# Kernel optimization log

Measured on AMD Instinct MI355X. Metric: run time of the kernel, lower is better.

The kernel has to match this reference:

```python
import jax, jax.numpy as jnp
import numpy as np
from jax import lax

B, S, N, C = 8, 256, 64, 64  # batch, time=freq (square, required by concat), n, c
EPS = 1e-3  # keras BatchNormalization / LayerNormalization default epsilon


def _conv(x, w, b):
    # 3x3 stride-1 SAME conv, NHWC / HWIO
    return lax.conv_general_dilated(x, w, (1, 1), 'SAME',
                                    dimension_numbers=('NHWC', 'HWIO', 'NHWC')) + b


def _bn(x, g, b):
    # training-mode batch norm: stats over batch+spatial axes
    m = jnp.mean(x, (0, 1, 2))
    v = jnp.var(x, (0, 1, 2))
    return (x - m) * lax.rsqrt(v + EPS) * g + b


def _ln(x, g, b):
    m = jnp.mean(x, -1, keepdims=True)
    v = jnp.var(x, -1, keepdims=True)
    return (x - m) * lax.rsqrt(v + EPS) * g + b


def _attn(q, k, v):
    # q,k,v: [B, C, L, D]; scaled dot-product attention over axis L
    d = q.shape[-1]
    s = jnp.einsum('bcid,bcjd->bcij', q, k) / jnp.sqrt(jnp.float32(d))
    a = jax.nn.softmax(s, axis=-1)
    return jnp.einsum('bcij,bcjd->bcid', a, v)


def setup_inputs():
    key = jax.random.key(0)
    ks = jax.random.split(key, 16)
    w = lambda k, sh: jax.random.normal(k, sh, jnp.float32) * 0.05
    inp = {
        'inputs': jax.random.normal(ks[0], (B, S, S, N), jnp.float32),
        'wq': w(ks[1], (3, 3, N, C)), 'bq': jnp.zeros((C,), jnp.float32),
        'wk': w(ks[2], (3, 3, N, C)), 'bk': jnp.zeros((C,), jnp.float32),
        'wv': w(ks[3], (3, 3, N, C)), 'bv': jnp.zeros((C,), jnp.float32),
        'gq': jnp.ones((C,), jnp.float32), 'betaq': jnp.zeros((C,), jnp.float32),
        'gk': jnp.ones((C,), jnp.float32), 'betak': jnp.zeros((C,), jnp.float32),
        'gv': jnp.ones((C,), jnp.float32), 'betav': jnp.zeros((C,), jnp.float32),
        'wc': w(ks[4], (3, 3, 2 * S, N)), 'bc': jnp.zeros((N,), jnp.float32),
        'ln_g': jnp.ones((N,), jnp.float32), 'ln_b': jnp.zeros((N,), jnp.float32),
        'w1': w(ks[5], (3, 3, N, N)), 'b1': jnp.zeros((N,), jnp.float32),
        'g1': jnp.ones((N,), jnp.float32), 'beta1': jnp.zeros((N,), jnp.float32),
        'w2': w(ks[6], (3, 3, N, N)), 'b2': jnp.zeros((N,), jnp.float32),
        'g2': jnp.ones((N,), jnp.float32), 'beta2': jnp.zeros((N,), jnp.float32),
    }
    return inp


def reference(inputs, wq, bq, wk, bk, wv, bv, gq, betaq, gk, betak, gv, betav,
              wc, bc, ln_g, ln_b, w1, b1, g1, beta1, w2, b2, g2, beta2):
    q = _bn(_conv(inputs, wq, bq), gq, betaq)
    k = _bn(_conv(inputs, wk, bk), gk, betak)
    v = _bn(_conv(inputs, wv, bv), gv, betav)
    # axial attention: over time ([B,C,T,F]) and over frequency ([B,C,F,T])
    qt, kt, vt = (jnp.transpose(t, (0, 3, 1, 2)) for t in (q, k, v))
    qf, kf, vf = (jnp.transpose(t, (0, 3, 2, 1)) for t in (q, k, v))
    at = _attn(qt, kt, vt)  # [B, C, S, S]
    af = _attn(qf, kf, vf)  # [B, C, S, S]
    out = jnp.concatenate([at, af], axis=-1)  # [B, C, S, 2S] treated as NHWC
    out = _ln(_conv(out, wc, bc), ln_g, ln_b)  # [B, C, S, N]
    f1 = _bn(jax.nn.relu(_conv(out, w1, b1)), g1, beta1)
    f2 = _bn(jax.nn.relu(_conv(f1, w2, b2)), g2, beta2)
    return f2
```

## Files before the change

kernel.cpp:

```cpp
#include <hip/hip_runtime.h>
#include <hip/hip_bf16.h>

typedef unsigned short u16;
typedef u16 us8 __attribute__((ext_vector_type(8)));
typedef u16 us4 __attribute__((ext_vector_type(4)));
typedef __bf16 bfx8 __attribute__((ext_vector_type(8)));
typedef float f32x4 __attribute__((ext_vector_type(4)));

#define EPS 1e-3f

__device__ __forceinline__ float bf2f(u16 u){ unsigned x = ((unsigned)u)<<16; return __builtin_bit_cast(float, x); }
__device__ __forceinline__ u16 f2bu(float f){ __hip_bfloat16 h = __float2bfloat16(f); return __builtin_bit_cast(u16, h); }
__device__ __forceinline__ bfx8 ldb8(const u16* p){ return __builtin_bit_cast(bfx8, *(const us8*)p); }

__global__ __launch_bounds__(256) void prepw_k(const float* __restrict__ src, u16* __restrict__ dst, int CI)
{
  int total = 9*CI*64;
  int idx = blockIdx.x*256 + threadIdx.x;
  if (idx < total){
    int ci = idx % CI; int rest = idx / CI; int co = rest & 63; int t = rest >> 6;
    dst[idx] = f2bu(src[((size_t)t*CI + ci)*64 + co]);
  }
}

__global__ __launch_bounds__(768) void conv_qkv_f32_k(
    const float* __restrict__ in,
    const u16* __restrict__ WtQ, const u16* __restrict__ WtK, const u16* __restrict__ WtV,
    const float* __restrict__ bq, const float* __restrict__ bk, const float* __restrict__ bv,
    u16* __restrict__ qo, u16* __restrict__ ko, u16* __restrict__ vo)
{
  int b = blockIdx.z, y0 = blockIdx.y*2, x0 = blockIdx.x*128;
  int tid = threadIdx.x, lane = tid & 63, wid = tid >> 6;
  int g3 = wid >> 2, wid4 = wid & 3;
  int l15 = lane & 15, lhi = lane >> 4;
  __shared__ u16 lds[4*130*64];

  for (int idx = tid; idx < 8320; idx += 768){
    int row = idx >> 4, c4 = idx & 15;
    int yy = row / 130, xx = row - yy*130;
    int gy = y0 + yy - 1, gx = x0 + xx - 1;
    us4 v = {0,0,0,0};
    if ((unsigned)gy < 256u && (unsigned)gx < 256u){
      float4 f = *(const float4*)(in + ((((size_t)b*256 + gy)*256 + gx)<<6) + c4*4);
      v[0] = f2bu(f.x); v[1] = f2bu(f.y); v[2] = f2bu(f.z); v[3] = f2bu(f.w);
    }
    *(us4*)(lds + row*64 + ((c4*4) ^ ((xx&7)<<3))) = v;
  }
  __syncthreads();

  const u16*  Wt   = (g3==0) ? WtQ : (g3==1) ? WtK : WtV;
  const float* bias = (g3==0) ? bq  : (g3==1) ? bk  : bv;
  u16*        outp = (g3==0) ? qo  : (g3==1) ? ko  : vo;

  f32x4 acc[2][2][4];
#pragma unroll
  for (int nf=0; nf<4; nf++){
    float bb = bias[nf*16 + l15];
#pragma unroll
    for (int ry=0; ry<2; ry++){
      acc[ry][0][nf] = (f32x4){bb,bb,bb,bb};
      acc[ry][1][nf] = (f32x4){bb,bb,bb,bb};
    }
  }
  int xbase = wid4*32;
#pragma unroll
  for (int ky=0; ky<3; ky++)
#pragma unroll
    for (int kx=0; kx<3; kx++){
      int t = ky*3 + kx;
      bfx8 bfr[2][4];
#pragma unroll
      for (int ks=0; ks<2; ks++)
#pragma unroll
        for (int nf=0; nf<4; nf++)
          bfr[ks][nf] = ldb8(Wt + ((t*64 + nf*16 + l15)<<6) + ks*32 + lhi*8);
#pragma unroll
      for (int ks=0; ks<2; ks++)
#pragma unroll
        for (int ry=0; ry<2; ry++)
#pragma unroll
          for (int mt=0; mt<2; mt++){
            int xx = xbase + mt*16 + l15 + kx;
            bfx8 a = ldb8(lds + ((ry+ky)*130 + xx)*64 + ((ks*32 + lhi*8) ^ ((xx&7)<<3)));
#pragma unroll
            for (int nf=0; nf<4; nf++)
              acc[ry][mt][nf] = __builtin_amdgcn_mfma_f32_16x16x32_bf16(a, bfr[ks][nf], acc[ry][mt][nf], 0,0,0);
          }
    }
#pragma unroll
  for (int ry=0; ry<2; ry++)
#pragma unroll
    for (int mt=0; mt<2; mt++)
#pragma unroll
      for (int nf=0; nf<4; nf++)
#pragma unroll
        for (int r=0; r<4; r++){
          int x = x0 + xbase + mt*16 + lhi*4 + r;
          outp[((((size_t)b*256 + (y0+ry))*256 + x)<<6) + nf*16 + l15] = f2bu(acc[ry][mt][nf][r]);
        }
}

template<bool RELU>
__global__ __launch_bounds__(256) void conv2_mfma_k(
    const u16* __restrict__ in, const u16* __restrict__ Wt, const float* __restrict__ bias,
    u16* __restrict__ out)
{
  int b = blockIdx.z, y0 = blockIdx.y*2, x0 = blockIdx.x*128;
  int tid = threadIdx.x, lane = tid & 63, wid = tid >> 6;
  int l15 = lane & 15, lhi = lane >> 4;
  __shared__ u16 lds[4*130*64];

  for (int idx = tid; idx < 4160; idx += 256){
    int row = idx >> 3, ch = idx & 7;
    int yy = row / 130, xx = row - yy*130;
    int gy = y0 + yy - 1, gx = x0 + xx - 1;
    us8 v = {0,0,0,0,0,0,0,0};
    if ((unsigned)gy < 64u && (unsigned)gx < 256u)
      v = *(const us8*)(in + ((((size_t)b*64 + gy)*256 + gx)<<6) + ch*8);
    *(us8*)(lds + row*64 + ((ch*8) ^ ((xx&7)<<3))) = v;
  }
  __syncthreads();

  f32x4 acc[2][2][4];
#pragma unroll
  for (int nf=0; nf<4; nf++){
    float bb = bias[nf*16 + l15];
#pragma unroll
    for (int ry=0; ry<2; ry++){
      acc[ry][0][nf] = (f32x4){bb,bb,bb,bb};
      acc[ry][1][nf] = (f32x4){bb,bb,bb,bb};
    }
  }
  int xbase = wid*32;
#pragma unroll
  for (int ky=0; ky<3; ky++)
#pragma unroll
    for (int kx=0; kx<3; kx++){
      int t = ky*3 + kx;
      bfx8 bfr[2][4];
#pragma unroll
      for (int ks=0; ks<2; ks++)
#pragma unroll
        for (int nf=0; nf<4; nf++)
          bfr[ks][nf] = ldb8(Wt + ((t*64 + nf*16 + l15)<<6) + ks*32 + lhi*8);
#pragma unroll
      for (int ks=0; ks<2; ks++)
#pragma unroll
        for (int ry=0; ry<2; ry++)
#pragma unroll
          for (int mt=0; mt<2; mt++){
            int xx = xbase + mt*16 + l15 + kx;
            bfx8 a = ldb8(lds + ((ry+ky)*130 + xx)*64 + ((ks*32 + lhi*8) ^ ((xx&7)<<3)));
#pragma unroll
            for (int nf=0; nf<4; nf++)
              acc[ry][mt][nf] = __builtin_amdgcn_mfma_f32_16x16x32_bf16(a, bfr[ks][nf], acc[ry][mt][nf], 0,0,0);
          }
    }
#pragma unroll
  for (int ry=0; ry<2; ry++)
#pragma unroll
    for (int mt=0; mt<2; mt++)
#pragma unroll
      for (int nf=0; nf<4; nf++)
#pragma unroll
        for (int r=0; r<4; r++){
          int x = x0 + xbase + mt*16 + lhi*4 + r;
          float vv = acc[ry][mt][nf][r];
          if (RELU) vv = fmaxf(vv, 0.f);
          out[((((size_t)b*64 + (y0+ry))*256 + x)<<6) + nf*16 + l15] = f2bu(vv);
        }
}

__global__ __launch_bounds__(256) void conv_cat_ln_k(
    const u16* __restrict__ in, const u16* __restrict__ Wt, const float* __restrict__ bias,
    const float* __restrict__ lng, const float* __restrict__ lnb, u16* __restrict__ out)
{
  int b = blockIdx.z, y0 = blockIdx.y*2, x0 = blockIdx.x*128;
  int tid = threadIdx.x, lane = tid & 63, wid = tid >> 6;
  int l15 = lane & 15, lhi = lane >> 4;
  __shared__ u16 lds[4*130*64];

  f32x4 acc[2][2][4];
#pragma unroll
  for (int nf=0; nf<4; nf++){
    float bb = bias[nf*16 + l15];
#pragma unroll
    for (int ry=0; ry<2; ry++){
      acc[ry][0][nf] = (f32x4){bb,bb,bb,bb};
      acc[ry][1][nf] = (f32x4){bb,bb,bb,bb};
    }
  }
  int xbase = wid*32;
  for (int ci0 = 0; ci0 < 512; ci0 += 64){
    __syncthreads();
    for (int idx = tid; idx < 4160; idx += 256){
      int row = idx >> 3, ch = idx & 7;
      int yy = row / 130, xx = row - yy*130;
      int gy = y0 + yy - 1, gx = x0 + xx - 1;
      us8 v = {0,0,0,0,0,0,0,0};
      if ((unsigned)gy < 64u && (unsigned)gx < 256u)
        v = *(const us8*)(in + ((((size_t)b*64 + gy)*256 + gx)<<9) + ci0 + ch*8);
      *(us8*)(lds + row*64 + ((ch*8) ^ ((xx&7)<<3))) = v;
    }
    __syncthreads();
#pragma unroll
    for (int ky=0; ky<3; ky++)
#pragma unroll
      for (int kx=0; kx<3; kx++){
        int t = ky*3 + kx;
        bfx8 bfr[2][4];
#pragma unroll
        for (int ks=0; ks<2; ks++)
#pragma unroll
          for (int nf=0; nf<4; nf++)
            bfr[ks][nf] = ldb8(Wt + ((size_t)(t*64 + nf*16 + l15)<<9) + ci0 + ks*32 + lhi*8);
#pragma unroll
        for (int ks=0; ks<2; ks++)
#pragma unroll
          for (int ry=0; ry<2; ry++)
#pragma unroll
            for (int mt=0; mt<2; mt++){
              int xx = xbase + mt*16 + l15 + kx;
              bfx8 a = ldb8(lds + ((ry+ky)*130 + xx)*64 + ((ks*32 + lhi*8) ^ ((xx&7)<<3)));
#pragma unroll
              for (int nf=0; nf<4; nf++)
                acc[ry][mt][nf] = __builtin_amdgcn_mfma_f32_16x16x32_bf16(a, bfr[ks][nf], acc[ry][mt][nf], 0,0,0);
            }
      }
  }
  float lg[4], lb[4];
#pragma unroll
  for (int nf=0; nf<4; nf++){ lg[nf] = lng[nf*16+l15]; lb[nf] = lnb[nf*16+l15]; }
#pragma unroll
  for (int ry=0; ry<2; ry++)
#pragma unroll
    for (int mt=0; mt<2; mt++)
#pragma unroll
      for (int r=0; r<4; r++){
        float v0 = acc[ry][mt][0][r], v1 = acc[ry][mt][1][r], v2 = acc[ry][mt][2][r], v3 = acc[ry][mt][3][r];
        float s = v0+v1+v2+v3;
        s += __shfl_xor(s,1); s += __shfl_xor(s,2); s += __shfl_xor(s,4); s += __shfl_xor(s,8);
        float m = s * 0.015625f;
        float d0=v0-m, d1=v1-m, d2=v2-m, d3=v3-m;
        float q = d0*d0+d1*d1+d2*d2+d3*d3;
        q += __shfl_xor(q,1); q += __shfl_xor(q,2); q += __shfl_xor(q,4); q += __shfl_xor(q,8);
        float rs = rsqrtf(q*0.015625f + EPS);
        int x = x0 + xbase + mt*16 + lhi*4 + r;
        size_t base = ((((size_t)b*64 + (y0+ry))*256 + x)<<6) + l15;
        out[base]    = f2bu(d0*rs*lg[0] + lb[0]);
        out[base+16] = f2bu(d1*rs*lg[1] + lb[1]);
        out[base+32] = f2bu(d2*rs*lg[2] + lb[2]);
        out[base+48] = f2bu(d3*rs*lg[3] + lb[3]);
      }
}

__global__ __launch_bounds__(256) void stats_k(const u16* __restrict__ x, size_t n4,
                                               float* __restrict__ partial)
{
  int tid = threadIdx.x;
  float s[4] = {0,0,0,0}, q[4] = {0,0,0,0};
  for (size_t i = (size_t)blockIdx.x*256 + tid; i < n4; i += (size_t)256*1024){
    us4 u = ((const us4*)x)[i];
#pragma unroll
    for (int e=0; e<4; e++){ float v = bf2f(u[e]); s[e] += v; q[e] += v*v; }
  }
  __shared__ float sm[256][8];
#pragma unroll
  for (int e=0; e<4; e++){ sm[tid][e] = s[e]; sm[tid][4+e] = q[e]; }
  __syncthreads();
  for (int st = 128; st >= 16; st >>= 1){
    if (tid < st)
#pragma unroll
      for (int e=0; e<8; e++) sm[tid][e] += sm[tid+st][e];
    __syncthreads();
  }
  if (tid < 16){
    int c0 = tid*4;
#pragma unroll
    for (int e=0; e<4; e++){
      partial[(size_t)blockIdx.x*128 + c0 + e]      = sm[tid][e];
      partial[(size_t)blockIdx.x*128 + 64 + c0 + e] = sm[tid][4+e];
    }
  }
}

__global__ __launch_bounds__(256) void finalize_k(const float* __restrict__ partial,
                                                  const float* __restrict__ g, const float* __restrict__ beta,
                                                  float inv_count, float* __restrict__ ss)
{
  __shared__ float sm[4][128];
  int c = threadIdx.x & 63, qq = threadIdx.x >> 6;
  float s = 0.f, v = 0.f;
  for (int i = qq*256; i < qq*256+256; i++){ s += partial[i*128 + c]; v += partial[i*128 + 64 + c]; }
  sm[qq][c] = s; sm[qq][64+c] = v;
  __syncthreads();
  if (qq == 0){
    s = sm[0][c]+sm[1][c]+sm[2][c]+sm[3][c];
    v = sm[0][64+c]+sm[1][64+c]+sm[2][64+c]+sm[3][64+c];
    float m = s*inv_count;
    float var = v*inv_count - m*m;
    float sc = g[c]*rsqrtf(var + EPS);
    ss[c] = sc; ss[64+c] = beta[c] - m*sc;
  }
}

__global__ __launch_bounds__(256) void bn_tr_k(const u16* __restrict__ x, const float* __restrict__ ss,
                                               u16* __restrict__ xT)
{
  int b = blockIdx.z, t = blockIdx.y, f0 = blockIdx.x*64;
  __shared__ float sm[64][65];
  int tid = threadIdx.x;
  for (int idx = tid; idx < 4096; idx += 256){
    int ci = idx & 63, fi = idx >> 6;
    float v = bf2f(x[((((size_t)b*256 + t)*256 + f0 + fi)<<6) + ci]);
    sm[fi][ci] = v*ss[ci] + ss[64+ci];
  }
  __syncthreads();
  for (int idx = tid; idx < 4096; idx += 256){
    int fi = idx & 63, ci = idx >> 6;
    xT[(((size_t)b*64 + ci)<<16) + t*256 + f0 + fi] = f2bu(sm[fi][ci]);
  }
}

template<bool TRA, bool TRB>
__global__ __launch_bounds__(256) void gemm_k(const u16* __restrict__ A, const u16* __restrict__ B,
                                              u16* __restrict__ C, float scale,
                                              int ldC, size_t cBatch, int cOff)
{
  int bc = blockIdx.z;
  const u16* Ab = A + ((size_t)bc<<16);
  const u16* Bb = B + ((size_t)bc<<16);
  u16* Cb = C + (size_t)bc*cBatch + cOff;
  int i0 = blockIdx.y*128, j0 = blockIdx.x*128;
  int tid = threadIdx.x, lane = tid & 63, wid = tid >> 6;
  int l15 = lane & 15, lhi = lane >> 4;
  __shared__ u16 Al[128*64], Bl[128*64];
  f32x4 acc[2][8] = {};

  for (int k0 = 0; k0 < 256; k0 += 64){
    __syncthreads();
    if (!TRA){
      for (int idx = tid; idx < 1024; idx += 256){
        int r = idx >> 3, c8 = idx & 7;
        us8 v = *(const us8*)(Ab + (size_t)(i0+r)*256 + k0 + c8*8);
        *(us8*)(Al + r*64 + ((c8*8) ^ ((r&7)<<3))) = v;
      }
    } else {
      for (int idx = tid; idx < 1024; idx += 256){
        int kr = idx >> 4, c8 = idx & 15;
        us8 v = *(const us8*)(Ab + (size_t)(k0+kr)*256 + i0 + c8*8);
#pragma unroll
        for (int e=0; e<8; e++){
          int i = c8*8 + e;
          Al[i*64 + (kr ^ ((i&7)<<3))] = v[e];
        }
      }
    }
    if (!TRB){
      for (int idx = tid; idx < 1024; idx += 256){
        int r = idx >> 3, c8 = idx & 7;
        us8 v = *(const us8*)(Bb + (size_t)(j0+r)*256 + k0 + c8*8);
        *(us8*)(Bl + r*64 + ((c8*8) ^ ((r&7)<<3))) = v;
      }
    } else {
      for (int idx = tid; idx < 1024; idx += 256){
        int kr = idx >> 4, c8 = idx & 15;
        us8 v = *(const us8*)(Bb + (size_t)(k0+kr)*256 + j0 + c8*8);
#pragma unroll
        for (int e=0; e<8; e++){
          int j = c8*8 + e;
          Bl[j*64 + (kr ^ ((j&7)<<3))] = v[e];
        }
      }
    }
    __syncthreads();
    int wrow = wid*32;
#pragma unroll
    for (int ks=0; ks<2; ks++){
      bfx8 bfr[8];
#pragma unroll
      for (int nf=0; nf<8; nf++)
        bfr[nf] = ldb8(Bl + (nf*16+l15)*64 + ((ks*32 + lhi*8) ^ ((l15&7)<<3)));
#pragma unroll
      for (int mt=0; mt<2; mt++){
        int r = wrow + mt*16 + l15;
        bfx8 a = ldb8(Al + r*64 + ((ks*32 + lhi*8) ^ ((r&7)<<3)));
#pragma unroll
        for (int nf=0; nf<8; nf++)
          acc[mt][nf] = __builtin_amdgcn_mfma_f32_16x16x32_bf16(a, bfr[nf], acc[mt][nf], 0,0,0);
      }
    }
  }
#pragma unroll
  for (int mt=0; mt<2; mt++)
#pragma unroll
    for (int nf=0; nf<8; nf++)
#pragma unroll
      for (int r=0; r<4; r++){
        int i = i0 + wid*32 + mt*16 + lhi*4 + r;
        int j = j0 + nf*16 + l15;
        Cb[(size_t)i*ldC + j] = f2bu(acc[mt][nf][r]*scale);
      }
}

__global__ __launch_bounds__(256) void softmax_k(u16* __restrict__ P)
{
  size_t row = (size_t)blockIdx.x*4 + (threadIdx.x >> 6);
  int lane = threadIdx.x & 63;
  u16* p = P + row*256 + lane*4;
  us4 u = *(us4*)p;
  float v[4];
#pragma unroll
  for (int e=0; e<4; e++) v[e] = bf2f(u[e]);
  float m = fmaxf(fmaxf(v[0],v[1]), fmaxf(v[2],v[3]));
  for (int off=1; off<64; off<<=1) m = fmaxf(m, __shfl_xor(m, off));
  float s = 0.f;
#pragma unroll
  for (int e=0; e<4; e++){ v[e] = __expf(v[e]-m); s += v[e]; }
  for (int off=1; off<64; off<<=1) s += __shfl_xor(s, off);
  float inv = 1.f/s;
  us4 o;
#pragma unroll
  for (int e=0; e<4; e++) o[e] = f2bu(v[e]*inv);
  *(us4*)p = o;
}

__global__ __launch_bounds__(256) void apply_bn_b_k(const u16* __restrict__ x, const float* __restrict__ ss,
                                                    u16* __restrict__ out, int n4)
{
  int i = blockIdx.x*256 + threadIdx.x;
  if (i < n4){
    int c0 = (i & 15)*4;
    us4 u = ((const us4*)x)[i];
    us4 o;
#pragma unroll
    for (int e=0; e<4; e++) o[e] = f2bu(bf2f(u[e])*ss[c0+e] + ss[64+c0+e]);
    ((us4*)out)[i] = o;
  }
}

__global__ __launch_bounds__(256) void apply_bn_f_k(const u16* __restrict__ x, const float* __restrict__ ss,
                                                    float* __restrict__ out, int n4)
{
  int i = blockIdx.x*256 + threadIdx.x;
  if (i < n4){
    int c0 = (i & 15)*4;
    us4 u = ((const us4*)x)[i];
    float4 o;
    o.x = bf2f(u[0])*ss[c0]   + ss[64+c0];
    o.y = bf2f(u[1])*ss[c0+1] + ss[64+c0+1];
    o.z = bf2f(u[2])*ss[c0+2] + ss[64+c0+2];
    o.w = bf2f(u[3])*ss[c0+3] + ss[64+c0+3];
    ((float4*)out)[i] = o;
  }
}

extern "C" void kernel_launch(void* const* d_in, const int* in_sizes, int n_in,
                              void* d_out, int out_size, void* d_ws, size_t ws_size,
                              hipStream_t stream)
{
  const float* in    = (const float*)d_in[0];
  const float* wq    = (const float*)d_in[1];  const float* bq    = (const float*)d_in[2];
  const float* wk    = (const float*)d_in[3];  const float* bk    = (const float*)d_in[4];
  const float* wv    = (const float*)d_in[5];  const float* bv    = (const float*)d_in[6];
  const float* gq    = (const float*)d_in[7];  const float* betaq = (const float*)d_in[8];
  const float* gk    = (const float*)d_in[9];  const float* betak = (const float*)d_in[10];
  const float* gv    = (const float*)d_in[11]; const float* betav = (const float*)d_in[12];
  const float* wc    = (const float*)d_in[13]; const float* bcv   = (const float*)d_in[14];
  const float* lng   = (const float*)d_in[15]; const float* lnb   = (const float*)d_in[16];
  const float* w1    = (const float*)d_in[17]; const float* b1    = (const float*)d_in[18];
  const float* g1    = (const float*)d_in[19]; const float* beta1 = (const float*)d_in[20];
  const float* w2    = (const float*)d_in[21]; const float* b2    = (const float*)d_in[22];
  const float* g2    = (const float*)d_in[23]; const float* beta2 = (const float*)d_in[24];
  float* out = (float*)d_out;

  char* ws = (char*)d_ws;
  const size_t MB = 1ull<<20;
  u16* qraw = (u16*)(ws);
  u16* kraw = (u16*)(ws + 64*MB);
  u16* vraw = (u16*)(ws + 128*MB);
  u16* qT   = (u16*)(ws + 192*MB);
  u16* kT   = (u16*)(ws + 256*MB);
  u16* vT   = (u16*)(ws + 320*MB);
  u16* P1   = qraw;
  u16* P2   = kraw;
  u16* cat  = qT;
  u16* y0   = (u16*)(ws + 128*MB);
  u16* f1   = (u16*)(ws + 144*MB);
  u16* rr   = (u16*)(ws + 160*MB);
  float* partial = (float*)(ws + 384*MB);
  float* ssq = (float*)(ws + 384*MB + 524288);
  float* ssk = ssq + 128;  float* ssv = ssq + 256;
  float* ss1 = ssq + 384;  float* ss2 = ssq + 512;
  u16* wqT = (u16*)(ws + 384*MB + 524288 + 4096);
  u16* wkT = wqT + 36864; u16* wvT = wkT + 36864;
  u16* w1T = wvT + 36864; u16* w2T = w1T + 36864;
  u16* wcT = w2T + 36864;

  dim3 blk(256);
  dim3 blk768(768);

  prepw_k<<<144, blk, 0, stream>>>(wq, wqT, 64);
  prepw_k<<<144, blk, 0, stream>>>(wk, wkT, 64);
  prepw_k<<<144, blk, 0, stream>>>(wv, wvT, 64);
  prepw_k<<<144, blk, 0, stream>>>(w1, w1T, 64);
  prepw_k<<<144, blk, 0, stream>>>(w2, w2T, 64);
  prepw_k<<<1152, blk, 0, stream>>>(wc, wcT, 512);

  const float invN1 = 1.f/524288.f;
  conv_qkv_f32_k<<<dim3(2,128,8), blk768, 0, stream>>>(in, wqT,wkT,wvT, bq,bk,bv, qraw,kraw,vraw);
  stats_k<<<1024, blk, 0, stream>>>(qraw, 8388608ull, partial);
  finalize_k<<<1, blk, 0, stream>>>(partial, gq, betaq, invN1, ssq);
  bn_tr_k<<<dim3(4,256,8), blk, 0, stream>>>(qraw, ssq, qT);
  stats_k<<<1024, blk, 0, stream>>>(kraw, 8388608ull, partial);
  finalize_k<<<1, blk, 0, stream>>>(partial, gk, betak, invN1, ssk);
  bn_tr_k<<<dim3(4,256,8), blk, 0, stream>>>(kraw, ssk, kT);
  stats_k<<<1024, blk, 0, stream>>>(vraw, 8388608ull, partial);
  finalize_k<<<1, blk, 0, stream>>>(partial, gv, betav, invN1, ssv);
  bn_tr_k<<<dim3(4,256,8), blk, 0, stream>>>(vraw, ssv, vT);

  gemm_k<false,false><<<dim3(2,2,512), blk, 0, stream>>>(qT, kT, P1, 0.0625f, 256, 65536, 0);
  gemm_k<true ,true ><<<dim3(2,2,512), blk, 0, stream>>>(qT, kT, P2, 0.0625f, 256, 65536, 0);
  softmax_k<<<65536, blk, 0, stream>>>(P1);
  gemm_k<false,true ><<<dim3(2,2,512), blk, 0, stream>>>(P1, vT, cat, 1.f, 512, 131072, 0);
  gemm_k<false,false><<<dim3(2,2,512), blk, 0, stream>>>(P2, vT, cat, 1.f, 512, 131072, 256);

  conv_cat_ln_k<<<dim3(2,32,8), blk, 0, stream>>>(cat, wcT, bcv, lng, lnb, y0);

  const float invN2 = 1.f/131072.f;
  conv2_mfma_k<true><<<dim3(2,32,8), blk, 0, stream>>>(y0, w1T, b1, rr);
  stats_k<<<1024, blk, 0, stream>>>(rr, 2097152ull, partial);
  finalize_k<<<1, blk, 0, stream>>>(partial, g1, beta1, invN2, ss1);
  apply_bn_b_k<<<8192, blk, 0, stream>>>(rr, ss1, f1, 2097152);

  conv2_mfma_k<true><<<dim3(2,32,8), blk, 0, stream>>>(f1, w2T, b2, rr);
  stats_k<<<1024, blk, 0, stream>>>(rr, 2097152ull, partial);
  finalize_k<<<1, blk, 0, stream>>>(partial, g2, beta2, invN2, ss2);
  apply_bn_f_k<<<8192, blk, 0, stream>>>(rr, ss2, out, 2097152);
}
```

Measured before the change: 1.249 ms.

## Batch q/k/v BN stats and transpose; fold BN1 into second conv's load

```diff
diff --git a/kernel.cpp b/kernel.cpp
--- a/kernel.cpp
+++ b/kernel.cpp
@@ -100,24 +100,37 @@
         }
 }
 
-template<bool RELU>
+template<bool RELU, bool BNIN>
 __global__ __launch_bounds__(256) void conv2_mfma_k(
     const u16* __restrict__ in, const u16* __restrict__ Wt, const float* __restrict__ bias,
-    u16* __restrict__ out)
+    const float* __restrict__ ssin, u16* __restrict__ out)
 {
   int b = blockIdx.z, y0 = blockIdx.y*2, x0 = blockIdx.x*128;
   int tid = threadIdx.x, lane = tid & 63, wid = tid >> 6;
   int l15 = lane & 15, lhi = lane >> 4;
   __shared__ u16 lds[4*130*64];
+  __shared__ float ssm[128];
+  if (BNIN){
+    if (tid < 128) ssm[tid] = ssin[tid];
+    __syncthreads();
+  }
 
   for (int idx = tid; idx < 4160; idx += 256){
     int row = idx >> 3, ch = idx & 7;
     int yy = row / 130, xx = row - yy*130;
     int gy = y0 + yy - 1, gx = x0 + xx - 1;
-    us8 v = {0,0,0,0,0,0,0,0};
-    if ((unsigned)gy < 64u && (unsigned)gx < 256u)
-      v = *(const us8*)(in + ((((size_t)b*64 + gy)*256 + gx)<<6) + ch*8);
-    *(us8*)(lds + row*64 + ((ch*8) ^ ((xx&7)<<3))) = v;
+    us8 w = {0,0,0,0,0,0,0,0};
+    if ((unsigned)gy < 64u && (unsigned)gx < 256u){
+      us8 v = *(const us8*)(in + ((((size_t)b*64 + gy)*256 + gx)<<6) + ch*8);
+      if (BNIN){
+#pragma unroll
+        for (int e=0; e<8; e++){
+          int ci = ch*8 + e;
+          w[e] = f2bu(bf2f(v[e])*ssm[ci] + ssm[64+ci]);
+        }
+      } else w = v;
+    }
+    *(us8*)(lds + row*64 + ((ch*8) ^ ((xx&7)<<3))) = w;
   }
   __syncthreads();
 
@@ -254,6 +267,43 @@
       }
 }
 
+__global__ __launch_bounds__(256) void stats3_k(const u16* __restrict__ x, float* __restrict__ partial)
+{
+  int tid = threadIdx.x;
+  const us4* xv = (const us4*)x;
+  float s[3][4] = {}, q[3][4] = {};
+  for (size_t i = (size_t)blockIdx.x*256 + tid; i < 8388608ull; i += (size_t)256*1024){
+#pragma unroll
+    for (int tt=0; tt<3; tt++){
+      us4 u = xv[(size_t)tt*8388608 + i];
+#pragma unroll
+      for (int e=0; e<4; e++){ float v = bf2f(u[e]); s[tt][e] += v; q[tt][e] += v*v; }
+    }
+  }
+  __shared__ float sm[256][8];
+#pragma unroll
+  for (int tt=0; tt<3; tt++){
+    if (tt) __syncthreads();
+#pragma unroll
+    for (int e=0; e<4; e++){ sm[tid][e] = s[tt][e]; sm[tid][4+e] = q[tt][e]; }
+    __syncthreads();
+    for (int st = 128; st >= 16; st >>= 1){
+      if (tid < st)
+#pragma unroll
+        for (int e=0; e<8; e++) sm[tid][e] += sm[tid+st][e];
+      __syncthreads();
+    }
+    if (tid < 16){
+      int c0 = tid*4;
+#pragma unroll
+      for (int e=0; e<4; e++){
+        partial[(size_t)tt*131072 + (size_t)blockIdx.x*128 + c0 + e]      = sm[tid][e];
+        partial[(size_t)tt*131072 + (size_t)blockIdx.x*128 + 64 + c0 + e] = sm[tid][4+e];
+      }
+    }
+  }
+}
+
 __global__ __launch_bounds__(256) void stats_k(const u16* __restrict__ x, size_t n4,
                                                float* __restrict__ partial)
 {
@@ -281,6 +331,33 @@
       partial[(size_t)blockIdx.x*128 + c0 + e]      = sm[tid][e];
       partial[(size_t)blockIdx.x*128 + 64 + c0 + e] = sm[tid][4+e];
     }
+  }
+}
+
+__global__ __launch_bounds__(256) void finalize3_k(const float* __restrict__ partial,
+    const float* __restrict__ gq, const float* __restrict__ bq,
+    const float* __restrict__ gk, const float* __restrict__ bk,
+    const float* __restrict__ gv, const float* __restrict__ bv,
+    float inv_count, float* __restrict__ ssbase)
+{
+  int tt = blockIdx.x;
+  const float* part = partial + (size_t)tt*131072;
+  const float* g  = (tt==0)?gq:(tt==1)?gk:gv;
+  const float* be = (tt==0)?bq:(tt==1)?bk:bv;
+  float* ss = ssbase + tt*128;
+  __shared__ float sm[4][128];
+  int c = threadIdx.x & 63, qq = threadIdx.x >> 6;
+  float s = 0.f, v = 0.f;
+  for (int i = qq*256; i < qq*256+256; i++){ s += part[i*128 + c]; v += part[i*128 + 64 + c]; }
+  sm[qq][c] = s; sm[qq][64+c] = v;
+  __syncthreads();
+  if (qq == 0){
+    s = sm[0][c]+sm[1][c]+sm[2][c]+sm[3][c];
+    v = sm[0][64+c]+sm[1][64+c]+sm[2][64+c]+sm[3][64+c];
+    float m = s*inv_count;
+    float var = v*inv_count - m*m;
+    float sc = g[c]*rsqrtf(var + EPS);
+    ss[c] = sc; ss[64+c] = be[c] - m*sc;
   }
 }
 
@@ -304,21 +381,33 @@
   }
 }
 
-__global__ __launch_bounds__(256) void bn_tr_k(const u16* __restrict__ x, const float* __restrict__ ss,
-                                               u16* __restrict__ xT)
-{
-  int b = blockIdx.z, t = blockIdx.y, f0 = blockIdx.x*64;
+__global__ __launch_bounds__(256) void bn_tr3_k(const u16* __restrict__ xbase,
+                                                const float* __restrict__ ssbase,
+                                                u16* __restrict__ xTbase)
+{
+  int z = blockIdx.z, tt = z >> 3, b = z & 7;
+  const u16* x = xbase + (size_t)tt*33554432;
+  const float* ss = ssbase + tt*128;
+  u16* xT = xTbase + (size_t)tt*33554432;
+  int t = blockIdx.y, f0 = blockIdx.x*64;
   __shared__ float sm[64][65];
   int tid = threadIdx.x;
-  for (int idx = tid; idx < 4096; idx += 256){
-    int ci = idx & 63, fi = idx >> 6;
-    float v = bf2f(x[((((size_t)b*256 + t)*256 + f0 + fi)<<6) + ci]);
-    sm[fi][ci] = v*ss[ci] + ss[64+ci];
+  for (int idx = tid; idx < 512; idx += 256){
+    int fi = idx >> 3, cg = idx & 7;
+    us8 v = *(const us8*)(x + ((((size_t)b*256 + t)*256 + f0 + fi)<<6) + cg*8);
+#pragma unroll
+    for (int e=0; e<8; e++){
+      int ci = cg*8 + e;
+      sm[fi][ci] = bf2f(v[e])*ss[ci] + ss[64+ci];
+    }
   }
   __syncthreads();
-  for (int idx = tid; idx < 4096; idx += 256){
-    int fi = idx & 63, ci = idx >> 6;
-    xT[(((size_t)b*64 + ci)<<16) + t*256 + f0 + fi] = f2bu(sm[fi][ci]);
+  for (int idx = tid; idx < 512; idx += 256){
+    int ci = idx >> 3, fg = idx & 7;
+    us8 o;
+#pragma unroll
+    for (int e=0; e<8; e++) o[e] = f2bu(sm[fg*8+e][ci]);
+    *(us8*)(xT + (((size_t)b*64 + ci)<<16) + t*256 + f0 + fg*8) = o;
   }
 }
 
@@ -423,20 +512,6 @@
 #pragma unroll
   for (int e=0; e<4; e++) o[e] = f2bu(v[e]*inv);
   *(us4*)p = o;
-}
-
-__global__ __launch_bounds__(256) void apply_bn_b_k(const u16* __restrict__ x, const float* __restrict__ ss,
-                                                    u16* __restrict__ out, int n4)
-{
-  int i = blockIdx.x*256 + threadIdx.x;
-  if (i < n4){
-    int c0 = (i & 15)*4;
-    us4 u = ((const us4*)x)[i];
-    us4 o;
-#pragma unroll
-    for (int e=0; e<4; e++) o[e] = f2bu(bf2f(u[e])*ss[c0+e] + ss[64+c0+e]);
-    ((us4*)out)[i] = o;
-  }
 }
 
 __global__ __launch_bounds__(256) void apply_bn_f_k(const u16* __restrict__ x, const float* __restrict__ ss,
@@ -488,11 +563,10 @@
   u16* y0   = (u16*)(ws + 128*MB);
   u16* f1   = (u16*)(ws + 144*MB);
   u16* rr   = (u16*)(ws + 160*MB);
-  float* partial = (float*)(ws + 384*MB);
-  float* ssq = (float*)(ws + 384*MB + 524288);
-  float* ssk = ssq + 128;  float* ssv = ssq + 256;
+  float* partial = (float*)(ws + 352*MB);
+  float* ssq = (float*)(ws + 384*MB);
   float* ss1 = ssq + 384;  float* ss2 = ssq + 512;
-  u16* wqT = (u16*)(ws + 384*MB + 524288 + 4096);
+  u16* wqT = (u16*)(ws + 384*MB + 4096);
   u16* wkT = wqT + 36864; u16* wvT = wkT + 36864;
   u16* w1T = wvT + 36864; u16* w2T = w1T + 36864;
   u16* wcT = w2T + 36864;
@@ -509,15 +583,9 @@
 
   const float invN1 = 1.f/524288.f;
   conv_qkv_f32_k<<<dim3(2,128,8), blk768, 0, stream>>>(in, wqT,wkT,wvT, bq,bk,bv, qraw,kraw,vraw);
-  stats_k<<<1024, blk, 0, stream>>>(qraw, 8388608ull, partial);
-  finalize_k<<<1, blk, 0, stream>>>(partial, gq, betaq, invN1, ssq);
-  bn_tr_k<<<dim3(4,256,8), blk, 0, stream>>>(qraw, ssq, qT);
-  stats_k<<<1024, blk, 0, stream>>>(kraw, 8388608ull, partial);
-  finalize_k<<<1, blk, 0, stream>>>(partial, gk, betak, invN1, ssk);
-  bn_tr_k<<<dim3(4,256,8), blk, 0, stream>>>(kraw, ssk, kT);
-  stats_k<<<1024, blk, 0, stream>>>(vraw, 8388608ull, partial);
-  finalize_k<<<1, blk, 0, stream>>>(partial, gv, betav, invN1, ssv);
-  bn_tr_k<<<dim3(4,256,8), blk, 0, stream>>>(vraw, ssv, vT);
+  stats3_k<<<1024, blk, 0, stream>>>(qraw, partial);
+  finalize3_k<<<3, blk, 0, stream>>>(partial, gq,betaq, gk,betak, gv,betav, invN1, ssq);
+  bn_tr3_k<<<dim3(4,256,24), blk, 0, stream>>>(qraw, ssq, qT);
 
   gemm_k<false,false><<<dim3(2,2,512), blk, 0, stream>>>(qT, kT, P1, 0.0625f, 256, 65536, 0);
   gemm_k<true ,true ><<<dim3(2,2,512), blk, 0, stream>>>(qT, kT, P2, 0.0625f, 256, 65536, 0);
@@ -528,13 +596,12 @@
   conv_cat_ln_k<<<dim3(2,32,8), blk, 0, stream>>>(cat, wcT, bcv, lng, lnb, y0);
 
   const float invN2 = 1.f/131072.f;
-  conv2_mfma_k<true><<<dim3(2,32,8), blk, 0, stream>>>(y0, w1T, b1, rr);
+  conv2_mfma_k<true,false><<<dim3(2,32,8), blk, 0, stream>>>(y0, w1T, b1, ssq, rr);
   stats_k<<<1024, blk, 0, stream>>>(rr, 2097152ull, partial);
   finalize_k<<<1, blk, 0, stream>>>(partial, g1, beta1, invN2, ss1);
-  apply_bn_b_k<<<8192, blk, 0, stream>>>(rr, ss1, f1, 2097152);
-
-  conv2_mfma_k<true><<<dim3(2,32,8), blk, 0, stream>>>(f1, w2T, b2, rr);
-  stats_k<<<1024, blk, 0, stream>>>(rr, 2097152ull, partial);
+
+  conv2_mfma_k<true,true><<<dim3(2,32,8), blk, 0, stream>>>(rr, w2T, b2, ss1, f1);
+  stats_k<<<1024, blk, 0, stream>>>(f1, 2097152ull, partial);
   finalize_k<<<1, blk, 0, stream>>>(partial, g2, beta2, invN2, ss2);
-  apply_bn_f_k<<<8192, blk, 0, stream>>>(rr, ss2, out, 2097152);
-}
+  apply_bn_f_k<<<8192, blk, 0, stream>>>(f1, ss2, out, 2097152);
+}
```

Result: faster. 1.210 ms (-3.1%).
